# Optimization experiments

Hardware: AMD Instinct MI355X
Metric: run time of the kernel (lower is better)

## Reference

```python
import jax, jax.numpy as jnp
import numpy as np
from jax import lax

B, HIST, FC, N, F = 64, 24, 24, 1000, 8
EMB, HID, NEMB, OUT = 32, 64, 1000, 1
IN = EMB + OUT  # GRU input dim


def setup_inputs() -> dict:
    key = jax.random.key(0)
    ks = jax.random.split(key, 11)
    X = jax.random.normal(ks[0], (B, HIST + FC, N, F), jnp.float32)
    idx = jax.random.randint(ks[1], (B, HIST + FC, N), 0, NEMB)
    X = X.at[..., -1].set(idx.astype(jnp.float32))  # last channel = spatial ids
    hn = jax.random.normal(ks[2], (B * N, HID), jnp.float32)
    xn = jax.random.normal(ks[3], (B, N, OUT), jnp.float32)
    s = 0.1
    emb_table = jax.random.normal(ks[4], (NEMB, EMB), jnp.float32) * s
    W_ih = jax.random.normal(ks[5], (3 * HID, IN), jnp.float32) * s
    W_hh = jax.random.normal(ks[6], (3 * HID, HID), jnp.float32) * s
    b_ih = jax.random.normal(ks[7], (3 * HID,), jnp.float32) * s
    b_hh = jax.random.normal(ks[8], (3 * HID,), jnp.float32) * s
    W_out = jax.random.normal(ks[9], (OUT, HID), jnp.float32) * s
    b_out = jax.random.normal(ks[10], (OUT,), jnp.float32) * s
    return {"X": X, "hn": hn, "xn": xn, "emb_table": emb_table,
            "W_ih": W_ih, "W_hh": W_hh, "b_ih": b_ih, "b_hh": b_hh,
            "W_out": W_out, "b_out": b_out}


def reference(X, hn, xn, emb_table, W_ih, W_hh, b_ih, b_hh, W_out, b_out):
    # indices for the forecast steps: [FC, B, N]
    idx_seq = X[:, :FC, :, -1].astype(jnp.int32).transpose(1, 0, 2)

    def step(carry, idx_t):
        h, x_prev = carry                      # h: [B*N, HID], x_prev: [B, N, 1]
        emb = emb_table[idx_t]                 # [B, N, EMB] gather
        x = jnp.concatenate([x_prev, emb], axis=-1).reshape(B * N, IN)
        gi = x @ W_ih.T + b_ih                 # [B*N, 3*HID]
        gh = h @ W_hh.T + b_hh
        i_r, i_z, i_n = jnp.split(gi, 3, axis=-1)
        h_r, h_z, h_n = jnp.split(gh, 3, axis=-1)
        r = jax.nn.sigmoid(i_r + h_r)
        z = jax.nn.sigmoid(i_z + h_z)
        n = jnp.tanh(i_n + r * h_n)
        h_new = (1.0 - z) * n + z * h
        out = h_new.reshape(B, N, HID) @ W_out.T + b_out  # [B, N, 1]
        return (h_new, out), out

    _, preds = lax.scan(step, (hn, xn), idx_seq)  # preds: [FC, B, N, 1]
    return preds.transpose(1, 0, 2, 3)            # [B, FC, N, 1]
```

## Files before the change

kernel.cpp:

```cpp
#include <hip/hip_runtime.h>
#include <math.h>

#define BB   64
#define FC   24
#define NN   1000
#define HID  64
#define EMBD 32
#define TT   48
#define FF   8
#define NEMB 1000
#define G3   192
#define INSZ 33

#define CPB  64
#define TPB  256
#define AST  72

typedef __attribute__((ext_vector_type(8))) short bf16x8;
typedef __attribute__((ext_vector_type(4))) float f32x4;

static __device__ __forceinline__ unsigned short f2bf(float f) {
    unsigned u = __builtin_bit_cast(unsigned, f);
    u += 0x7FFFu + ((u >> 16) & 1u);
    return (unsigned short)(u >> 16);
}
static __device__ __forceinline__ float fast_sigmoid(float v) {
    float e = __builtin_amdgcn_exp2f(-1.4426950408889634f * v);
    return __builtin_amdgcn_rcpf(1.0f + e);
}
static __device__ __forceinline__ float fast_tanh(float v) {
    float vv = fminf(fmaxf(v, -15.0f), 15.0f);
    float e = __builtin_amdgcn_exp2f(2.8853900817779268f * vv);
    return 1.0f - 2.0f * __builtin_amdgcn_rcpf(e + 1.0f);
}

__global__ __launch_bounds__(G3) void premul_kernel(
    const float* __restrict__ emb, const float* __restrict__ Wih,
    const float* __restrict__ bih, const float* __restrict__ bhh,
    float* __restrict__ P3)
{
    __shared__ float xe[EMBD];
    const int e = blockIdx.x;
    const int j = threadIdx.x;
    if (j < EMBD) xe[j] = emb[e * EMBD + j];
    __syncthreads();
    float acc = bih[j] + (j < 2 * HID ? bhh[j] : 0.0f);
    const float* w = Wih + (size_t)j * INSZ + 1;
    #pragma unroll
    for (int k = 0; k < EMBD; ++k) acc = fmaf(w[k], xe[k], acc);
    P3[(size_t)e * G3 + (j & 63) * 3 + (j >> 6)] = acc;
}

__global__ __launch_bounds__(TPB) void gru_decoder(
    const float* __restrict__ X,
    const float* __restrict__ hn0,
    const float* __restrict__ xn,
    const float* __restrict__ Whh,
    const float* __restrict__ bhh,
    const float* __restrict__ Wih,
    const float* __restrict__ Wout,
    const float* __restrict__ bout,
    const float* __restrict__ P3,
    float* __restrict__ out)
{
    __shared__ __align__(16) unsigned short Abuf[CPB * AST];
    __shared__ int   idxbuf[FC * CPB];
    __shared__ float xbuf[CPB];
    __shared__ float obuf[4 * CPB];
    __shared__ float Woutlds[HID];

    const int tid  = threadIdx.x;
    const int lane = tid & 63;
    const int g    = tid >> 6;
    const int quad = lane >> 4;
    const int l15  = lane & 15;
    const int jcol = g * 16 + l15;
    const int rowb = quad * 4;

    for (int e = tid; e < FC * CPB; e += TPB) {
        int t  = e >> 6;
        int cl = e & 63;
        int cell = blockIdx.x * CPB + cl;
        int b = cell / NN, n = cell - b * NN;
        idxbuf[e] = (int)X[(((size_t)b * TT + t) * NN + n) * FF + 7];
    }
    if (tid < CPB) {
        int cell = blockIdx.x * CPB + tid;
        xbuf[tid] = xn[cell];
        Woutlds[tid] = Wout[tid];
    }

    bf16x8 Bf[3][2];
    #pragma unroll
    for (int gate = 0; gate < 3; ++gate) {
        #pragma unroll
        for (int ks = 0; ks < 2; ++ks) {
            const float* src = Whh + (size_t)(gate * HID + jcol) * HID + ks * 32 + quad * 8;
            float4 lo = *(const float4*)src;
            float4 hi = *(const float4*)(src + 4);
            bf16x8 f;
            f[0] = (short)f2bf(lo.x); f[1] = (short)f2bf(lo.y);
            f[2] = (short)f2bf(lo.z); f[3] = (short)f2bf(lo.w);
            f[4] = (short)f2bf(hi.x); f[5] = (short)f2bf(hi.y);
            f[6] = (short)f2bf(hi.z); f[7] = (short)f2bf(hi.w);
            Bf[gate][ks] = f;
        }
    }

    const float w0r = Wih[(size_t)jcol * INSZ];
    const float w0z = Wih[(size_t)(HID + jcol) * INSZ];
    const float w0n = Wih[(size_t)(2 * HID + jcol) * INSZ];
    const float bhn = bhh[2 * HID + jcol];
    const float bout0 = bout[0];

    float hold[4][4];
    #pragma unroll
    for (int mt = 0; mt < 4; ++mt) {
        #pragma unroll
        for (int rr = 0; rr < 4; ++rr) {
            int m = mt * 16 + rowb + rr;
            float h = hn0[((size_t)blockIdx.x * CPB + m) * HID + jcol];
            hold[mt][rr] = h;
            Abuf[m * AST + jcol] = f2bf(h);
        }
    }
    __syncthreads();

    for (int t = 0; t < FC; ++t) {
        f32x4 accr[4], accz[4], accn[4];
        #pragma unroll
        for (int mt = 0; mt < 4; ++mt) {
            const bf16x8 a0 = *(const bf16x8*)&Abuf[(mt * 16 + l15) * AST + quad * 8];
            const bf16x8 a1 = *(const bf16x8*)&Abuf[(mt * 16 + l15) * AST + 32 + quad * 8];
            f32x4 z4 = {0.f, 0.f, 0.f, 0.f};
            accr[mt] = __builtin_amdgcn_mfma_f32_16x16x32_bf16(a0, Bf[0][0], z4, 0, 0, 0);
            accr[mt] = __builtin_amdgcn_mfma_f32_16x16x32_bf16(a1, Bf[0][1], accr[mt], 0, 0, 0);
            accz[mt] = __builtin_amdgcn_mfma_f32_16x16x32_bf16(a0, Bf[1][0], z4, 0, 0, 0);
            accz[mt] = __builtin_amdgcn_mfma_f32_16x16x32_bf16(a1, Bf[1][1], accz[mt], 0, 0, 0);
            accn[mt] = __builtin_amdgcn_mfma_f32_16x16x32_bf16(a0, Bf[2][0], z4, 0, 0, 0);
            accn[mt] = __builtin_amdgcn_mfma_f32_16x16x32_bf16(a1, Bf[2][1], accn[mt], 0, 0, 0);
        }
        __syncthreads();

        #pragma unroll
        for (int mt = 0; mt < 4; ++mt) {
            #pragma unroll
            for (int rr = 0; rr < 4; ++rr) {
                int m   = mt * 16 + rowb + rr;
                int idx = idxbuf[t * CPB + m];
                float xp = xbuf[m];
                const float* pp = P3 + (size_t)idx * G3 + jcol * 3;
                float ar = fmaf(w0r, xp, pp[0]);
                float az = fmaf(w0z, xp, pp[1]);
                float an = fmaf(w0n, xp, pp[2]);
                float r  = fast_sigmoid(ar + accr[mt][rr]);
                float z  = fast_sigmoid(az + accz[mt][rr]);
                float nv = fast_tanh(an + r * (accn[mt][rr] + bhn));
                float hnew = nv + z * (hold[mt][rr] - nv);
                hold[mt][rr] = hnew;
                Abuf[m * AST + jcol] = f2bf(hnew);
            }
        }
        __syncthreads();

        {
            const int c = tid & 63;
            const int q = tid >> 6;
            float o = 0.f;
            #pragma unroll
            for (int e2 = 0; e2 < 8; ++e2) {
                unsigned v = *(const unsigned*)&Abuf[c * AST + q * 16 + 2 * e2];
                float hlo = __builtin_bit_cast(float, v << 16);
                float hhi = __builtin_bit_cast(float, v & 0xFFFF0000u);
                o = fmaf(Woutlds[q * 16 + 2 * e2],     hlo, o);
                o = fmaf(Woutlds[q * 16 + 2 * e2 + 1], hhi, o);
            }
            obuf[q * CPB + c] = o;
        }
        __syncthreads();

        if (tid < CPB) {
            int cell = blockIdx.x * CPB + tid;
            int b = cell / NN, n = cell - b * NN;
            float o = bout0 + obuf[tid] + obuf[CPB + tid]
                    + obuf[2 * CPB + tid] + obuf[3 * CPB + tid];
            out[((size_t)b * FC + t) * NN + n] = o;
            xbuf[tid] = o;
        }
        __syncthreads();
    }
}

extern "C" void kernel_launch(void* const* d_in, const int* in_sizes, int n_in,
                              void* d_out, int out_size, void* d_ws, size_t ws_size,
                              hipStream_t stream) {
    (void)in_sizes; (void)n_in; (void)out_size; (void)ws_size;
    const float* X    = (const float*)d_in[0];
    const float* hn   = (const float*)d_in[1];
    const float* xn   = (const float*)d_in[2];
    const float* emb  = (const float*)d_in[3];
    const float* Wih  = (const float*)d_in[4];
    const float* Whh  = (const float*)d_in[5];
    const float* bih  = (const float*)d_in[6];
    const float* bhh  = (const float*)d_in[7];
    const float* Wout = (const float*)d_in[8];
    const float* bout = (const float*)d_in[9];
    float* out = (float*)d_out;
    float* P3  = (float*)d_ws;

    premul_kernel<<<NEMB, G3, 0, stream>>>(emb, Wih, bih, bhh, P3);

    const int blocks = (BB * NN) / CPB;
    gru_decoder<<<blocks, TPB, 0, stream>>>(X, hn, xn, Whh, bhh, Wih,
                                            Wout, bout, P3, out);
}
```

Baseline: 293.5 us.

## Halve cells per block, fuse output projection into MFMA phase with shuffles

The decoder block drops from 64 to 32 cells, so 2000 blocks are launched instead of 1000 and each wave handles two M-tiles. The per-step output projection now runs through wave shuffle reductions and is deferred into the next step's MFMA phase. This removes two of the four barriers per timestep and the obuf/Woutlds shared buffers. Other changes: an occupancy hint (waves_per_eu 4), and premul now computes 8 embeddings per block from a transposed Wih staged in LDS, at the cost of each block reloading all of Wih.

```diff
diff --git a/kernel.cpp b/kernel.cpp
--- a/kernel.cpp
+++ b/kernel.cpp
@@ -12,9 +12,12 @@
 #define G3   192
 #define INSZ 33
 
-#define CPB  64
+#define CPB  32
 #define TPB  256
+#define MT   2
 #define AST  72
+
+#define EPB  8
 
 typedef __attribute__((ext_vector_type(8))) short bf16x8;
 typedef __attribute__((ext_vector_type(4))) float f32x4;
@@ -34,24 +37,38 @@
     return 1.0f - 2.0f * __builtin_amdgcn_rcpf(e + 1.0f);
 }
 
-__global__ __launch_bounds__(G3) void premul_kernel(
+__global__ __launch_bounds__(256) void premul_kernel(
     const float* __restrict__ emb, const float* __restrict__ Wih,
     const float* __restrict__ bih, const float* __restrict__ bhh,
     float* __restrict__ P3)
 {
-    __shared__ float xe[EMBD];
-    const int e = blockIdx.x;
-    const int j = threadIdx.x;
-    if (j < EMBD) xe[j] = emb[e * EMBD + j];
+    __shared__ float Wihs[INSZ * G3];
+    __shared__ float xes[EPB * EMBD];
+    const int tid = threadIdx.x;
+    const int e0  = blockIdx.x * EPB;
+
+    for (int i = tid; i < G3 * INSZ; i += 256) {
+        int j = i / INSZ, k = i - j * INSZ;
+        Wihs[k * G3 + j] = Wih[i];
+    }
+    xes[tid] = emb[(size_t)e0 * EMBD + tid];
     __syncthreads();
-    float acc = bih[j] + (j < 2 * HID ? bhh[j] : 0.0f);
-    const float* w = Wih + (size_t)j * INSZ + 1;
-    #pragma unroll
-    for (int k = 0; k < EMBD; ++k) acc = fmaf(w[k], xe[k], acc);
-    P3[(size_t)e * G3 + (j & 63) * 3 + (j >> 6)] = acc;
-}
-
-__global__ __launch_bounds__(TPB) void gru_decoder(
+
+    const int el = tid >> 5;
+    const float* xe = xes + el * EMBD;
+    #pragma unroll
+    for (int i = 0; i < G3 / 32; ++i) {
+        int j = (tid & 31) + 32 * i;
+        float acc = bih[j] + (j < 2 * HID ? bhh[j] : 0.0f);
+        #pragma unroll
+        for (int k = 0; k < EMBD; ++k)
+            acc = fmaf(Wihs[(k + 1) * G3 + j], xe[k], acc);
+        P3[(size_t)(e0 + el) * G3 + (j & 63) * 3 + (j >> 6)] = acc;
+    }
+}
+
+__global__ __launch_bounds__(TPB) __attribute__((amdgpu_waves_per_eu(4)))
+void gru_decoder(
     const float* __restrict__ X,
     const float* __restrict__ hn0,
     const float* __restrict__ xn,
@@ -66,8 +83,6 @@
     __shared__ __align__(16) unsigned short Abuf[CPB * AST];
     __shared__ int   idxbuf[FC * CPB];
     __shared__ float xbuf[CPB];
-    __shared__ float obuf[4 * CPB];
-    __shared__ float Woutlds[HID];
 
     const int tid  = threadIdx.x;
     const int lane = tid & 63;
@@ -76,19 +91,15 @@
     const int l15  = lane & 15;
     const int jcol = g * 16 + l15;
     const int rowb = quad * 4;
+    const int cell0 = blockIdx.x * CPB;
 
     for (int e = tid; e < FC * CPB; e += TPB) {
-        int t  = e >> 6;
-        int cl = e & 63;
-        int cell = blockIdx.x * CPB + cl;
+        int t = e >> 5, m = e & 31;
+        int cell = cell0 + m;
         int b = cell / NN, n = cell - b * NN;
-        idxbuf[e] = (int)X[(((size_t)b * TT + t) * NN + n) * FF + 7];
-    }
-    if (tid < CPB) {
-        int cell = blockIdx.x * CPB + tid;
-        xbuf[tid] = xn[cell];
-        Woutlds[tid] = Wout[tid];
-    }
+        idxbuf[t * CPB + m] = (int)X[(((size_t)b * TT + t) * NN + n) * FF + 7];
+    }
+    if (tid < CPB) xbuf[tid] = xn[cell0 + tid];
 
     bf16x8 Bf[3][2];
     #pragma unroll
@@ -113,13 +124,22 @@
     const float bhn = bhh[2 * HID + jcol];
     const float bout0 = bout[0];
 
-    float hold[4][4];
-    #pragma unroll
-    for (int mt = 0; mt < 4; ++mt) {
+    const int cd_m   = g * 8 + (lane & 7);
+    const int kslice = lane >> 3;
+    float wout_r[8];
+    #pragma unroll
+    for (int e2 = 0; e2 < 8; ++e2) wout_r[e2] = Wout[kslice * 8 + e2];
+    const int cd_cell = cell0 + cd_m;
+    const int cd_b = cd_cell / NN, cd_n = cd_cell - cd_b * NN;
+    const size_t obase = (size_t)cd_b * FC * NN + cd_n;
+
+    float hold[MT][4];
+    #pragma unroll
+    for (int mt = 0; mt < MT; ++mt) {
         #pragma unroll
         for (int rr = 0; rr < 4; ++rr) {
             int m = mt * 16 + rowb + rr;
-            float h = hn0[((size_t)blockIdx.x * CPB + m) * HID + jcol];
+            float h = hn0[((size_t)cell0 + m) * HID + jcol];
             hold[mt][rr] = h;
             Abuf[m * AST + jcol] = f2bf(h);
         }
@@ -127,9 +147,9 @@
     __syncthreads();
 
     for (int t = 0; t < FC; ++t) {
-        f32x4 accr[4], accz[4], accn[4];
-        #pragma unroll
-        for (int mt = 0; mt < 4; ++mt) {
+        f32x4 accr[MT], accz[MT], accn[MT];
+        #pragma unroll
+        for (int mt = 0; mt < MT; ++mt) {
             const bf16x8 a0 = *(const bf16x8*)&Abuf[(mt * 16 + l15) * AST + quad * 8];
             const bf16x8 a1 = *(const bf16x8*)&Abuf[(mt * 16 + l15) * AST + 32 + quad * 8];
             f32x4 z4 = {0.f, 0.f, 0.f, 0.f};
@@ -140,10 +160,30 @@
             accn[mt] = __builtin_amdgcn_mfma_f32_16x16x32_bf16(a0, Bf[2][0], z4, 0, 0, 0);
             accn[mt] = __builtin_amdgcn_mfma_f32_16x16x32_bf16(a1, Bf[2][1], accn[mt], 0, 0, 0);
         }
+
+        if (t > 0) {
+            bf16x8 hv = *(const bf16x8*)&Abuf[cd_m * AST + kslice * 8];
+            const unsigned* hv32 = (const unsigned*)&hv;
+            float o = 0.f;
+            #pragma unroll
+            for (int q = 0; q < 4; ++q) {
+                unsigned v = hv32[q];
+                o = fmaf(wout_r[2 * q],     __builtin_bit_cast(float, v << 16),         o);
+                o = fmaf(wout_r[2 * q + 1], __builtin_bit_cast(float, v & 0xFFFF0000u), o);
+            }
+            o += __shfl_xor(o, 8);
+            o += __shfl_xor(o, 16);
+            o += __shfl_xor(o, 32);
+            if (lane < 8) {
+                float oo = o + bout0;
+                out[obase + (size_t)(t - 1) * NN] = oo;
+                xbuf[cd_m] = oo;
+            }
+        }
         __syncthreads();
 
         #pragma unroll
-        for (int mt = 0; mt < 4; ++mt) {
+        for (int mt = 0; mt < MT; ++mt) {
             #pragma unroll
             for (int rr = 0; rr < 4; ++rr) {
                 int m   = mt * 16 + rowb + rr;
@@ -162,32 +202,22 @@
             }
         }
         __syncthreads();
-
-        {
-            const int c = tid & 63;
-            const int q = tid >> 6;
-            float o = 0.f;
-            #pragma unroll
-            for (int e2 = 0; e2 < 8; ++e2) {
-                unsigned v = *(const unsigned*)&Abuf[c * AST + q * 16 + 2 * e2];
-                float hlo = __builtin_bit_cast(float, v << 16);
-                float hhi = __builtin_bit_cast(float, v & 0xFFFF0000u);
-                o = fmaf(Woutlds[q * 16 + 2 * e2],     hlo, o);
-                o = fmaf(Woutlds[q * 16 + 2 * e2 + 1], hhi, o);
-            }
-            obuf[q * CPB + c] = o;
-        }
-        __syncthreads();
-
-        if (tid < CPB) {
-            int cell = blockIdx.x * CPB + tid;
-            int b = cell / NN, n = cell - b * NN;
-            float o = bout0 + obuf[tid] + obuf[CPB + tid]
-                    + obuf[2 * CPB + tid] + obuf[3 * CPB + tid];
-            out[((size_t)b * FC + t) * NN + n] = o;
-            xbuf[tid] = o;
-        }
-        __syncthreads();
+    }
+
+    {
+        bf16x8 hv = *(const bf16x8*)&Abuf[cd_m * AST + kslice * 8];
+        const unsigned* hv32 = (const unsigned*)&hv;
+        float o = 0.f;
+        #pragma unroll
+        for (int q = 0; q < 4; ++q) {
+            unsigned v = hv32[q];
+            o = fmaf(wout_r[2 * q],     __builtin_bit_cast(float, v << 16),         o);
+            o = fmaf(wout_r[2 * q + 1], __builtin_bit_cast(float, v & 0xFFFF0000u), o);
+        }
+        o += __shfl_xor(o, 8);
+        o += __shfl_xor(o, 16);
+        o += __shfl_xor(o, 32);
+        if (lane < 8) out[obase + (size_t)(FC - 1) * NN] = o + bout0;
     }
 }
 
@@ -208,7 +238,7 @@
     float* out = (float*)d_out;
     float* P3  = (float*)d_ws;
 
-    premul_kernel<<<NEMB, G3, 0, stream>>>(emb, Wih, bih, bhh, P3);
+    premul_kernel<<<NEMB / EPB, 256, 0, stream>>>(emb, Wih, bih, bhh, P3);
 
     const int blocks = (BB * NN) / CPB;
     gru_decoder<<<blocks, TPB, 0, stream>>>(X, hn, xn, Whh, bhh, Wih,
```

Measured after the change: 267.6 us. 8.8% less time.
